# Optimization experiments

Measured on AMD Instinct MI355X. Metric: run time of the kernel, lower is better.

The kernel has to match this reference:

```python
import jax, jax.numpy as jnp
import numpy as np

EPS = 1e-6
NUM_HEADS = 16  # config.num_attention_heads

def _rms(h, w):
    h32 = h.astype(jnp.float32)
    v = jnp.mean(h32 * h32, axis=-1, keepdims=True)
    return (w * h32 * jax.lax.rsqrt(v + EPS)).astype(h.dtype)

def _rope(q, k, pos):
    dh = q.shape[-1]
    inv = 1.0 / (10000.0 ** (jnp.arange(0, dh, 2, dtype=jnp.float32) / dh))
    ang = pos.astype(jnp.float32)[:, None] * inv[None, :]  # [n, dh/2]
    cos = jnp.concatenate([jnp.cos(ang), jnp.cos(ang)], -1)[None, None]  # [1,1,n,dh]
    sin = jnp.concatenate([jnp.sin(ang), jnp.sin(ang)], -1)[None, None]
    def rot(x):
        x1, x2 = x[..., :dh // 2], x[..., dh // 2:]
        return jnp.concatenate([-x2, x1], -1)
    return q * cos + rot(q) * sin, k * cos + rot(k) * sin

def _skip_causal_mask(N, block_size, len1, text_len):
    qi = jnp.arange(N)[:, None]
    ki = jnp.arange(N)[None, :]
    qb = (qi - text_len) // block_size
    kb = (ki - text_len) // block_size
    iq = qi >= text_len
    ik = ki >= text_len
    return (((ki < text_len) & (qi >= ki))
            | (iq & ik & (qb < len1) & (kb < len1) & (qb >= kb))
            | (iq & ik & (qb >= len1) & (kb < len1) & (qb - len1 > kb))
            | (iq & ik & (qb == kb)))

def _layer(x, position_ids, text_position_ids, qkv_w, qkv_b, proj_w, proj_b,
           qn_w, kn_w, ln1_w, ln2_w, gate_w, up_w, down_w,
           block_size, text_len, len1):
    B, N, C = x.shape
    H = NUM_HEADS
    Dh = C // H
    T = text_len
    Lc = len1 * block_size
    offs = [0, T, T + Lc]
    lens = [T, Lc, N - T - Lc]  # text / clean / noised segment lengths
    qs, ks, vs = [], [], []
    for i in range(3):
        seg = _rms(x[:, offs[i]:offs[i] + lens[i]], ln1_w[i])  # input layernorm
        qkv = seg @ qkv_w[i] + qkv_b[i]                        # [B,n,3C]
        qkv = qkv.reshape(B, lens[i], 3, H, Dh).transpose(2, 0, 3, 1, 4)
        qs.append(_rms(qkv[0], qn_w[i]))
        ks.append(_rms(qkv[1], kn_w[i]))
        vs.append(qkv[2])
    img_q = jnp.concatenate([qs[1], qs[2]], axis=2)
    img_k = jnp.concatenate([ks[1], ks[2]], axis=2)
    img_q, img_k = _rope(img_q, img_k, position_ids)
    txt_q, txt_k = _rope(qs[0], ks[0], text_position_ids)
    q = jnp.concatenate([txt_q, img_q], axis=2)
    k = jnp.concatenate([txt_k, img_k], axis=2)
    v = jnp.concatenate(vs, axis=2)
    scores = jnp.einsum('bhqd,bhkd->bhqk', q, k) / np.float32(np.sqrt(Dh))
    mask = _skip_causal_mask(N, block_size, len1, text_len)
    scores = jnp.where(mask, scores, jnp.finfo(scores.dtype).min)
    attn = jax.nn.softmax(scores, axis=-1)
    o = jnp.einsum('bhqk,bhkd->bhqd', attn, v)
    o = o.transpose(0, 2, 1, 3).reshape(B, N, C)
    o = jnp.concatenate([o[:, offs[i]:offs[i] + lens[i]] @ proj_w[i] + proj_b[i]
                         for i in range(3)], axis=1)
    h = x + o
    mlp = []
    for i in range(3):
        y = _rms(h[:, offs[i]:offs[i] + lens[i]], ln2_w[i])  # post-attn layernorm
        mlp.append((jax.nn.silu(y @ gate_w[i]) * (y @ up_w[i])) @ down_w[i])
    return h + jnp.concatenate(mlp, axis=1)

def setup_inputs():
    key = jax.random.key(0)
    ks = jax.random.split(key, 8)
    B, C, H, I = 2, 1024, 16, 4096
    block_size, text_len, len1, len2 = 128, 256, 4, 4
    N = text_len + (len1 + len2) * block_size  # 1280
    s = 0.02
    return {
        'x': jax.random.normal(ks[0], (B, N, C), jnp.float32),
        'position_ids': jnp.arange((len1 + len2) * block_size, dtype=jnp.int32),
        'text_position_ids': jnp.arange(text_len, dtype=jnp.int32),
        'qkv_w': jax.random.normal(ks[1], (3, C, 3 * C), jnp.float32) * s,
        'qkv_b': jnp.zeros((3, 3 * C), jnp.float32),
        'proj_w': jax.random.normal(ks[2], (3, C, C), jnp.float32) * s,
        'proj_b': jnp.zeros((3, C), jnp.float32),
        'qn_w': jnp.ones((3, C // H), jnp.float32),
        'kn_w': jnp.ones((3, C // H), jnp.float32),
        'ln1_w': jnp.ones((3, C), jnp.float32),
        'ln2_w': jnp.ones((3, C), jnp.float32),
        'gate_w': jax.random.normal(ks[3], (3, C, I), jnp.float32) * s,
        'up_w': jax.random.normal(ks[4], (3, C, I), jnp.float32) * s,
        'down_w': jax.random.normal(ks[5], (3, I, C), jnp.float32) * s,
        'block_size': block_size, 'text_len': text_len, 'len1': len1,
    }

def reference(x, position_ids, text_position_ids, qkv_w, qkv_b, proj_w, proj_b,
              qn_w, kn_w, ln1_w, ln2_w, gate_w, up_w, down_w,
              block_size, text_len, len1):
    return _layer(x, position_ids, text_position_ids, qkv_w, qkv_b, proj_w, proj_b,
                  qn_w, kn_w, ln1_w, ln2_w, gate_w, up_w, down_w,
                  block_size, text_len, len1)
```

## Files before the change

### kernel.cpp

```cpp
#include <hip/hip_runtime.h>
#include <math.h>

constexpr int Bb  = 2;
constexpr int Nn  = 1280;
constexpr int Cc  = 1024;
constexpr int Hh  = 16;
constexpr int DH  = 64;
constexpr int Ii  = 4096;
constexpr int Tt  = 256;
constexpr int BSz = 128;
constexpr int L1  = 4;
constexpr int Mrows = Bb * Nn;

typedef __attribute__((ext_vector_type(8))) short short8v;
typedef __attribute__((ext_vector_type(4))) float f32x4;

__device__ __forceinline__ int segof(int n) {
    return n < Tt ? 0 : (n < Tt + L1 * BSz ? 1 : 2);
}
__device__ __forceinline__ unsigned short f2bf(float f) {
    unsigned int u = __float_as_uint(f);
    u += 0x7fffu + ((u >> 16) & 1u);
    return (unsigned short)(u >> 16);
}
__device__ __forceinline__ float bf2f(unsigned short h) {
    return __uint_as_float(((unsigned int)h) << 16);
}

__device__ __forceinline__ int xcd_swz(int lin, int nwg) {
    int cpx = nwg >> 3;
    return (lin & 7) * cpx + (lin >> 3);
}

__global__ __launch_bounds__(256)
void rms_bf16(const float* __restrict__ in, const float* __restrict__ w,
              unsigned short* __restrict__ out) {
    int row = blockIdx.x;
    int n   = row % Nn;
    int seg = segof(n);
    const float* x = in + (size_t)row * Cc;
    int t = threadIdx.x;
    float4 xv = reinterpret_cast<const float4*>(x)[t];
    float ss = xv.x * xv.x + xv.y * xv.y + xv.z * xv.z + xv.w * xv.w;
#pragma unroll
    for (int off = 32; off; off >>= 1) ss += __shfl_down(ss, off, 64);
    __shared__ float red[4];
    __shared__ float s_r;
    int lane = t & 63, wid = t >> 6;
    if (lane == 0) red[wid] = ss;
    __syncthreads();
    if (t == 0) s_r = rsqrtf((red[0] + red[1] + red[2] + red[3]) * (1.0f / Cc) + 1e-6f);
    __syncthreads();
    float r = s_r;
    float4 wv = reinterpret_cast<const float4*>(w + (size_t)seg * Cc)[t];
    ushort4 ov;
    ov.x = f2bf(wv.x * xv.x * r);
    ov.y = f2bf(wv.y * xv.y * r);
    ov.z = f2bf(wv.z * xv.z * r);
    ov.w = f2bf(wv.w * xv.w * r);
    *reinterpret_cast<ushort4*>(&out[(size_t)row * Cc + t * 4]) = ov;
}

__global__ __launch_bounds__(256)
void pack_w(const float* __restrict__ W, unsigned short* __restrict__ PB,
            int K, int Nd) {
    size_t idx = (size_t)blockIdx.x * 256 + threadIdx.x;
    size_t cpseg = (size_t)K * Nd / 8;
    int s = (int)(idx / cpseg);
    size_t rm = idx % cpseg;
    int lane = (int)(rm & 63);
    int fr   = (int)((rm >> 6) & 7);
    size_t tile = rm >> 9;
    int nct = Nd >> 7;
    int cb = (int)(tile % nct);
    int kt = (int)(tile / nct);
    int col = cb * 128 + fr * 16 + (lane & 15);
    int k0  = kt * 32 + (lane >> 4) * 8;
    const float* src = W + ((size_t)s * K + k0) * Nd + col;
    unsigned short o[8];
#pragma unroll
    for (int j = 0; j < 8; j++) o[j] = f2bf(src[(size_t)j * Nd]);
    short8v v;
#pragma unroll
    for (int j = 0; j < 8; j++) v[j] = (short)o[j];
    *reinterpret_cast<short8v*>(&PB[idx * 8]) = v;
}

template <int OUTMODE, bool BIAS, int NZ>
__global__ __launch_bounds__(256, 2)
void gemm128r(const unsigned short* __restrict__ A,
              const unsigned short* __restrict__ PB,
              const float* __restrict__ bias, void* __restrict__ outp,
              int K, int Nd) {
    __shared__ __align__(16) unsigned short lds[8192];
    int bx = blockIdx.x, by = blockIdx.y, bz = (NZ > 1) ? blockIdx.z : 0;
    {
        int gx = gridDim.x, gy = gridDim.y, gz = (NZ > 1) ? gridDim.z : 1;
        int lin = bx + gx * (by + gy * bz);
        int swz = xcd_swz(lin, gx * gy * gz);
        bx = swz % gx; swz /= gx;
        by = swz % gy; bz = swz / gy;
    }
    int rb = bx * 128, cb = by;
    int seg = segof(rb % Nn);
    int tid = threadIdx.x, lane = tid & 63, wid = tid >> 6;
    int wr = wid >> 1, wc = wid & 1;
    int g = lane >> 4, c_ = lane & 15;
    const int nct = Nd >> 7;
    const int Keff = K / NZ;
    const int nKt = Keff >> 5;
    const int kz = bz * Keff;
    const unsigned short* PBseg = PB + (size_t)seg * K * Nd;

    int mf0 = tid >> 6, lc0 = tid & 63;
    const unsigned short* pA0 =
        A + (size_t)(rb + mf0 * 16 + (lc0 & 15)) * K + kz + (lc0 >> 4) * 8;
    const unsigned short* pA1 = pA0 + (size_t)64 * K;
    const unsigned short* pB0 =
        PBseg + (((size_t)(kz >> 5) * nct + cb) * 8 + mf0) * 512 + (size_t)lc0 * 8;
    const unsigned short* pB1 = pB0 + 2048;
    const size_t bstep = (size_t)nct * 4096;

    f32x4 acc[4][4];
#pragma unroll
    for (int m = 0; m < 4; m++)
#pragma unroll
        for (int n = 0; n < 4; n++) acc[m][n] = (f32x4){0.f, 0.f, 0.f, 0.f};

    short8v av[2], bv[2];
    av[0] = *reinterpret_cast<const short8v*>(pA0);
    av[1] = *reinterpret_cast<const short8v*>(pA1);
    bv[0] = *reinterpret_cast<const short8v*>(pB0);
    bv[1] = *reinterpret_cast<const short8v*>(pB1);
    pA0 += 32; pA1 += 32; pB0 += bstep; pB1 += bstep;

    for (int kt = 0; kt < nKt; ++kt) {
        __syncthreads();
        *reinterpret_cast<short8v*>(&lds[(size_t)tid * 8]) = av[0];
        *reinterpret_cast<short8v*>(&lds[(size_t)(tid + 256) * 8]) = av[1];
        *reinterpret_cast<short8v*>(&lds[4096 + (size_t)tid * 8]) = bv[0];
        *reinterpret_cast<short8v*>(&lds[4096 + (size_t)(tid + 256) * 8]) = bv[1];
        __syncthreads();
        if (kt + 1 < nKt) {
            av[0] = *reinterpret_cast<const short8v*>(pA0);
            av[1] = *reinterpret_cast<const short8v*>(pA1);
            bv[0] = *reinterpret_cast<const short8v*>(pB0);
            bv[1] = *reinterpret_cast<const short8v*>(pB1);
            pA0 += 32; pA1 += 32; pB0 += bstep; pB1 += bstep;
        }
        short8v afr[4], bfr[4];
#pragma unroll
        for (int m = 0; m < 4; m++)
            afr[m] = *reinterpret_cast<short8v*>(&lds[((wr * 4 + m) * 64 + lane) * 8]);
#pragma unroll
        for (int n = 0; n < 4; n++)
            bfr[n] = *reinterpret_cast<short8v*>(&lds[4096 + ((wc * 4 + n) * 64 + lane) * 8]);
#pragma unroll
        for (int m = 0; m < 4; m++)
#pragma unroll
            for (int n = 0; n < 4; n++)
                acc[m][n] = __builtin_amdgcn_mfma_f32_16x16x32_bf16(
                    afr[m], bfr[n], acc[m][n], 0, 0, 0);
    }

    float* outf = (float*)outp;
    unsigned short* outh = (unsigned short*)outp;
    size_t zoff = (NZ > 1) ? (size_t)bz * Mrows * Nd : 0;
#pragma unroll
    for (int n = 0; n < 4; n++) {
        int col = cb * 128 + wc * 64 + n * 16 + c_;
        float bvv = BIAS ? bias[(size_t)seg * Nd + col] : 0.f;
#pragma unroll
        for (int m = 0; m < 4; m++) {
#pragma unroll
            for (int r = 0; r < 4; r++) {
                int row = rb + wr * 64 + m * 16 + g * 4 + r;
                float v = acc[m][n][r] + bvv;
                if (OUTMODE == 0) outf[zoff + (size_t)row * Nd + col] = v;
                else              outh[zoff + (size_t)row * Nd + col] = f2bf(v);
            }
        }
    }
}

__global__ __launch_bounds__(256, 2)
void gemm_gu(const unsigned short* __restrict__ A,
             const unsigned short* __restrict__ PG,
             const unsigned short* __restrict__ PU,
             unsigned short* __restrict__ outp) {
    __shared__ __align__(16) unsigned short lds[12288];
    int bx = blockIdx.x, by = blockIdx.y;
    {
        int lin = bx + gridDim.x * by;
        int swz = xcd_swz(lin, gridDim.x * gridDim.y);
        bx = swz % gridDim.x; by = swz / gridDim.x;
    }
    int rb = bx * 128, cb = by;
    int seg = segof(rb % Nn);
    int tid = threadIdx.x, lane = tid & 63, wid = tid >> 6;
    int wr = wid >> 1, wc = wid & 1;
    int g = lane >> 4, c_ = lane & 15;
    const int nct = Ii >> 7;
    const unsigned short* PGseg = PG + (size_t)seg * Cc * Ii;
    const unsigned short* PUseg = PU + (size_t)seg * Cc * Ii;

    int mf0 = tid >> 6, lc0 = tid & 63;
    const unsigned short* pA0 =
        A + (size_t)(rb + mf0 * 16 + (lc0 & 15)) * Cc + (lc0 >> 4) * 8;
    const unsigned short* pA1 = pA0 + (size_t)64 * Cc;
    size_t boff = ((size_t)cb * 8 + mf0) * 512 + (size_t)lc0 * 8;
    const unsigned short* pG0 = PGseg + boff;
    const unsigned short* pG1 = pG0 + 2048;
    const unsigned short* pU0 = PUseg + boff;
    const unsigned short* pU1 = pU0 + 2048;
    const size_t bstep = (size_t)nct * 4096;

    f32x4 accG[4][4], accU[4][4];
#pragma unroll
    for (int m = 0; m < 4; m++)
#pragma unroll
        for (int n = 0; n < 4; n++) {
            accG[m][n] = (f32x4){0.f, 0.f, 0.f, 0.f};
            accU[m][n] = (f32x4){0.f, 0.f, 0.f, 0.f};
        }

    short8v av[2], gv[2], uv[2];
    av[0] = *reinterpret_cast<const short8v*>(pA0);
    av[1] = *reinterpret_cast<const short8v*>(pA1);
    gv[0] = *reinterpret_cast<const short8v*>(pG0);
    gv[1] = *reinterpret_cast<const short8v*>(pG1);
    uv[0] = *reinterpret_cast<const short8v*>(pU0);
    uv[1] = *reinterpret_cast<const short8v*>(pU1);
    pA0 += 32; pA1 += 32; pG0 += bstep; pG1 += bstep; pU0 += bstep; pU1 += bstep;

    const int nKt = Cc >> 5;
    for (int kt = 0; kt < nKt; ++kt) {
        __syncthreads();
        *reinterpret_cast<short8v*>(&lds[(size_t)tid * 8]) = av[0];
        *reinterpret_cast<short8v*>(&lds[(size_t)(tid + 256) * 8]) = av[1];
        *reinterpret_cast<short8v*>(&lds[4096 + (size_t)tid * 8]) = gv[0];
        *reinterpret_cast<short8v*>(&lds[4096 + (size_t)(tid + 256) * 8]) = gv[1];
        *reinterpret_cast<short8v*>(&lds[8192 + (size_t)tid * 8]) = uv[0];
        *reinterpret_cast<short8v*>(&lds[8192 + (size_t)(tid + 256) * 8]) = uv[1];
        __syncthreads();
        if (kt + 1 < nKt) {
            av[0] = *reinterpret_cast<const short8v*>(pA0);
            av[1] = *reinterpret_cast<const short8v*>(pA1);
            gv[0] = *reinterpret_cast<const short8v*>(pG0);
            gv[1] = *reinterpret_cast<const short8v*>(pG1);
            uv[0] = *reinterpret_cast<const short8v*>(pU0);
            uv[1] = *reinterpret_cast<const short8v*>(pU1);
            pA0 += 32; pA1 += 32; pG0 += bstep; pG1 += bstep; pU0 += bstep; pU1 += bstep;
        }
        short8v afr[4];
#pragma unroll
        for (int m = 0; m < 4; m++)
            afr[m] = *reinterpret_cast<short8v*>(&lds[((wr * 4 + m) * 64 + lane) * 8]);
        {
            short8v gfr[4];
#pragma unroll
            for (int n = 0; n < 4; n++)
                gfr[n] = *reinterpret_cast<short8v*>(&lds[4096 + ((wc * 4 + n) * 64 + lane) * 8]);
#pragma unroll
            for (int m = 0; m < 4; m++)
#pragma unroll
                for (int n = 0; n < 4; n++)
                    accG[m][n] = __builtin_amdgcn_mfma_f32_16x16x32_bf16(
                        afr[m], gfr[n], accG[m][n], 0, 0, 0);
        }
        {
            short8v ufr[4];
#pragma unroll
            for (int n = 0; n < 4; n++)
                ufr[n] = *reinterpret_cast<short8v*>(&lds[8192 + ((wc * 4 + n) * 64 + lane) * 8]);
#pragma unroll
            for (int m = 0; m < 4; m++)
#pragma unroll
                for (int n = 0; n < 4; n++)
                    accU[m][n] = __builtin_amdgcn_mfma_f32_16x16x32_bf16(
                        afr[m], ufr[n], accU[m][n], 0, 0, 0);
        }
    }

#pragma unroll
    for (int n = 0; n < 4; n++) {
        int col = cb * 128 + wc * 64 + n * 16 + c_;
#pragma unroll
        for (int m = 0; m < 4; m++) {
#pragma unroll
            for (int r = 0; r < 4; r++) {
                int row = rb + wr * 64 + m * 16 + g * 4 + r;
                float gval = accG[m][n][r], uval = accU[m][n][r];
                float t = gval / (1.f + __expf(-gval)) * uval;
                outp[(size_t)row * Ii + col] = f2bf(t);
            }
        }
    }
}

__global__ __launch_bounds__(256)
void combine_proj(const float* __restrict__ x, const float* __restrict__ bias,
                  const float* __restrict__ p, float* __restrict__ hb) {
    int i = blockIdx.x * 256 + threadIdx.x;
    int base = i * 4;
    int col = base % Cc;
    int n   = (base / Cc) % Nn;
    int seg = segof(n);
    float4 a = reinterpret_cast<const float4*>(x)[i];
    float4 b = *reinterpret_cast<const float4*>(&bias[(size_t)seg * Cc + col]);
    float4 p0 = reinterpret_cast<const float4*>(p)[i];
    float4 p1 = reinterpret_cast<const float4*>(p)[i + Mrows * Cc / 4];
    float4 r;
    r.x = a.x + b.x + p0.x + p1.x;
    r.y = a.y + b.y + p0.y + p1.y;
    r.z = a.z + b.z + p0.z + p1.z;
    r.w = a.w + b.w + p0.w + p1.w;
    reinterpret_cast<float4*>(hb)[i] = r;
}

__global__ __launch_bounds__(256)
void combine_down4(const unsigned short* __restrict__ p,
                   float* __restrict__ out) {
    int i = blockIdx.x * 256 + threadIdx.x;
    float4 a = reinterpret_cast<const float4*>(out)[i];
#pragma unroll
    for (int z = 0; z < 4; z++) {
        ushort4 u = *reinterpret_cast<const ushort4*>(&p[(size_t)z * Mrows * Cc + i * 4]);
        a.x += bf2f(u.x); a.y += bf2f(u.y); a.z += bf2f(u.z); a.w += bf2f(u.w);
    }
    reinterpret_cast<float4*>(out)[i] = a;
}

__global__ __launch_bounds__(256)
void split_rope(const unsigned short* __restrict__ qkv,
                const float* __restrict__ qn_w, const float* __restrict__ kn_w,
                const int* __restrict__ pos_ids, const int* __restrict__ tpos_ids,
                unsigned short* __restrict__ Q, unsigned short* __restrict__ K,
                unsigned short* __restrict__ V) {
    int row = blockIdx.x;
    int b = row / Nn, n = row % Nn;
    int seg = segof(n);
    int lane = threadIdx.x & 63, wid = threadIdx.x >> 6;
    int pos = (n < Tt) ? tpos_ids[n] : pos_ids[n - Tt];
    int j = lane & 31;
    float ang = (float)pos * exp2f(-(float)j * (13.287712379549449f / 32.f));
    float cv = cosf(ang), sv = sinf(ang);
    float qw = qn_w[seg * DH + lane], kw = kn_w[seg * DH + lane];
    for (int h = wid; h < Hh; h += 4) {
        const unsigned short* base = qkv + (size_t)row * (3 * Cc) + h * DH + lane;
        float q = bf2f(base[0]), k = bf2f(base[Cc]), v = bf2f(base[2 * Cc]);
        float qs = q * q, ks = k * k;
#pragma unroll
        for (int off = 32; off; off >>= 1) {
            qs += __shfl_xor(qs, off, 64);
            ks += __shfl_xor(ks, off, 64);
        }
        q = q * rsqrtf(qs * (1.f / DH) + 1e-6f) * qw;
        k = k * rsqrtf(ks * (1.f / DH) + 1e-6f) * kw;
        float qp = __shfl_xor(q, 32, 64);
        float kp = __shfl_xor(k, 32, 64);
        float qo = q * cv + ((lane < 32) ? -qp * sv : qp * sv);
        float ko = k * cv + ((lane < 32) ? -kp * sv : kp * sv);
        size_t oidx = ((size_t)(b * Hh + h) * Nn + n) * DH + lane;
        Q[oidx] = f2bf(qo);
        K[oidx] = f2bf(ko);
        V[oidx] = f2bf(v);
    }
}

__global__ __launch_bounds__(256)
void attn_mfma(const unsigned short* __restrict__ Qg,
               const unsigned short* __restrict__ Kg,
               const unsigned short* __restrict__ Vg,
               unsigned short* __restrict__ O) {
    __shared__ __align__(16) unsigned short k_lds[64 * 64];
    __shared__ __align__(16) unsigned short vt_lds[64 * 64];
    __shared__ __align__(16) unsigned short p_lds[4][16 * 64];

    int qt = blockIdx.x;
    int bh = blockIdx.y;
    int b = bh >> 4, h = bh & 15;
    int tid = threadIdx.x, lane = tid & 63, wid = tid >> 6;
    int g = lane >> 4, c = lane & 15;

    const size_t headoff = (size_t)bh * Nn * DH;
    int q0 = qt * 64;
    bool qtext = q0 < Tt;
    int qb = qtext ? 0 : (q0 - Tt) / BSz;

    int qrow_frag = q0 + wid * 16 + c;
    short8v aq[2];
#pragma unroll
    for (int kb = 0; kb < 2; kb++)
        aq[kb] = *reinterpret_cast<const short8v*>(
            &Qg[headoff + (size_t)qrow_frag * DH + kb * 32 + g * 8]);

    unsigned short* pbuf = &p_lds[wid][0];

    f32x4 o_[4];
#pragma unroll
    for (int nb = 0; nb < 4; nb++) o_[nb] = (f32x4){0.f, 0.f, 0.f, 0.f};
    float m_[4] = {-3.4e38f, -3.4e38f, -3.4e38f, -3.4e38f};
    float l_[4] = {0.f, 0.f, 0.f, 0.f};

    int tr = tid >> 2, tc = tid & 3;

    for (int kt = 0; kt < Nn / 64; kt++) {
        int kbase = kt * 64;
        bool vis, diag = false;
        if (qtext) {
            vis = (kbase <= q0);
            diag = (kbase == q0);
        } else if (kbase < Tt) {
            vis = true;
        } else {
            int kb = (kbase - Tt) / BSz;
            vis = (qb < L1) ? (kb <= qb)
                            : ((kb < L1 && qb - L1 > kb) || kb == qb);
        }
        if (!vis) continue;

        __syncthreads();
        {
            const unsigned short* ks = &Kg[headoff + (size_t)(kbase + tr) * DH];
            const unsigned short* vs = &Vg[headoff + (size_t)(kbase + tr) * DH];
#pragma unroll
            for (int i = 0; i < 2; i++) {
                int ch = tc + i * 4;
                short8v kv = *reinterpret_cast<const short8v*>(ks + ch * 8);
                int byte = (tr * 128 + ch * 16) ^ ((tr & 7) << 4);
                *reinterpret_cast<short8v*>((char*)k_lds + byte) = kv;
                short8v vv = *reinterpret_cast<const short8v*>(vs + ch * 8);
#pragma unroll
                for (int j = 0; j < 8; j++) {
                    int dh = ch * 8 + j;
                    int vbyte = (dh * 128 + tr * 2) ^ ((dh & 7) << 4);
                    *reinterpret_cast<unsigned short*>((char*)vt_lds + vbyte) =
                        (unsigned short)vv[j];
                }
            }
        }
        __syncthreads();

        f32x4 s_[4];
#pragma unroll
        for (int nb = 0; nb < 4; nb++) s_[nb] = (f32x4){0.f, 0.f, 0.f, 0.f};
#pragma unroll
        for (int nb = 0; nb < 4; nb++) {
            int kil = nb * 16 + c;
#pragma unroll
            for (int kb = 0; kb < 2; kb++) {
                int byte = (kil * 128 + kb * 64 + g * 16) ^ ((kil & 7) << 4);
                short8v bk = *reinterpret_cast<short8v*>((char*)k_lds + byte);
                s_[nb] = __builtin_amdgcn_mfma_f32_16x16x32_bf16(aq[kb], bk, s_[nb], 0, 0, 0);
            }
        }
#pragma unroll
        for (int nb = 0; nb < 4; nb++) {
#pragma unroll
            for (int r = 0; r < 4; r++) {
                float sv = s_[nb][r] * 0.125f;
                if (diag) {
                    int qrl = wid * 16 + g * 4 + r;
                    int kcl = nb * 16 + c;
                    if (qrl < kcl) sv = -3.4e38f;
                }
                s_[nb][r] = sv;
            }
        }
#pragma unroll
        for (int r = 0; r < 4; r++) {
            float mx = fmaxf(fmaxf(s_[0][r], s_[1][r]), fmaxf(s_[2][r], s_[3][r]));
#pragma unroll
            for (int off = 1; off <= 8; off <<= 1)
                mx = fmaxf(mx, __shfl_xor(mx, off, 64));
            float mn = fmaxf(m_[r], mx);
            float es = __expf(m_[r] - mn);
            m_[r] = mn;
            float pv[4];
            float rs = 0.f;
#pragma unroll
            for (int nb = 0; nb < 4; nb++) {
                pv[nb] = __expf(s_[nb][r] - mn);
                rs += pv[nb];
            }
#pragma unroll
            for (int off = 1; off <= 8; off <<= 1)
                rs += __shfl_xor(rs, off, 64);
            l_[r] = l_[r] * es + rs;
#pragma unroll
            for (int nb = 0; nb < 4; nb++) o_[nb][r] *= es;
            int qrl = g * 4 + r;
            int swz = (qrl & 7) << 4;
#pragma unroll
            for (int nb = 0; nb < 4; nb++) {
                int byte = (qrl * 128 + (nb * 16 + c) * 2) ^ swz;
                *reinterpret_cast<unsigned short*>((char*)pbuf + byte) = f2bf(pv[nb]);
            }
        }
        short8v aP[2];
#pragma unroll
        for (int kb = 0; kb < 2; kb++) {
            int byte = (c * 128 + kb * 64 + g * 16) ^ ((c & 7) << 4);
            aP[kb] = *reinterpret_cast<short8v*>((char*)pbuf + byte);
        }
#pragma unroll
        for (int nb = 0; nb < 4; nb++) {
            int dh = nb * 16 + c;
#pragma unroll
            for (int kb = 0; kb < 2; kb++) {
                int byte = (dh * 128 + kb * 64 + g * 16) ^ ((dh & 7) << 4);
                short8v bv = *reinterpret_cast<short8v*>((char*)vt_lds + byte);
                o_[nb] = __builtin_amdgcn_mfma_f32_16x16x32_bf16(aP[kb], bv, o_[nb], 0, 0, 0);
            }
        }
    }

    float inv_[4];
#pragma unroll
    for (int r = 0; r < 4; r++) inv_[r] = 1.f / l_[r];
#pragma unroll
    for (int nb = 0; nb < 4; nb++) {
        int col = h * DH + nb * 16 + c;
#pragma unroll
        for (int r = 0; r < 4; r++) {
            int row = q0 + wid * 16 + g * 4 + r;
            O[((size_t)b * Nn + row) * Cc + col] = f2bf(o_[nb][r] * inv_[r]);
        }
    }
}

extern "C" void kernel_launch(void* const* d_in, const int* in_sizes, int n_in,
                              void* d_out, int out_size, void* d_ws, size_t ws_size,
                              hipStream_t stream) {
    const float* x        = (const float*)d_in[0];
    const int*   pos_ids  = (const int*)d_in[1];
    const int*   tpos_ids = (const int*)d_in[2];
    const float* qkv_w    = (const float*)d_in[3];
    const float* qkv_b    = (const float*)d_in[4];
    const float* proj_w   = (const float*)d_in[5];
    const float* proj_b   = (const float*)d_in[6];
    const float* qn_w     = (const float*)d_in[7];
    const float* kn_w     = (const float*)d_in[8];
    const float* ln1_w    = (const float*)d_in[9];
    const float* ln2_w    = (const float*)d_in[10];
    const float* gate_w   = (const float*)d_in[11];
    const float* up_w     = (const float*)d_in[12];
    const float* down_w   = (const float*)d_in[13];
    float* out = (float*)d_out;
    char*  wsb = (char*)d_ws;

    unsigned short* WA  = (unsigned short*)(wsb);
    unsigned short* WB  = (unsigned short*)(wsb + 25165824);
    unsigned short* Tb  = (unsigned short*)(wsb + 50331648);
    unsigned short* P3  = (unsigned short*)(wsb + 71303168);
    unsigned short* Qbf = Tb;
    unsigned short* Kbf = Tb + 2621440;
    unsigned short* Vbf = Tb + 5242880;

    rms_bf16<<<Mrows, 256, 0, stream>>>(x, ln1_w, P3);
    pack_w<<<4608, 256, 0, stream>>>(qkv_w, WA, Cc, 3 * Cc);
    gemm128r<1, true, 1><<<dim3(Mrows / 128, 24), 256, 0, stream>>>(
        P3, WA, qkv_b, WB, Cc, 3 * Cc);
    split_rope<<<Mrows, 256, 0, stream>>>(WB, qn_w, kn_w, pos_ids, tpos_ids,
                                          Qbf, Kbf, Vbf);
    attn_mfma<<<dim3(Nn / 64, Bb * Hh), 256, 0, stream>>>(Qbf, Kbf, Vbf, P3);
    pack_w<<<1536, 256, 0, stream>>>(proj_w, WA, Cc, Cc);
    gemm128r<0, false, 2><<<dim3(Mrows / 128, 8, 2), 256, 0, stream>>>(
        P3, WA, nullptr, (float*)Tb, Cc, Cc);
    combine_proj<<<Mrows * Cc / 1024, 256, 0, stream>>>(x, proj_b, (float*)Tb, out);
    rms_bf16<<<Mrows, 256, 0, stream>>>(out, ln2_w, P3);
    pack_w<<<6144, 256, 0, stream>>>(gate_w, WA, Cc, Ii);
    pack_w<<<6144, 256, 0, stream>>>(up_w, WB, Cc, Ii);
    gemm_gu<<<dim3(Mrows / 128, 32), 256, 0, stream>>>(P3, WA, WB, Tb);
    pack_w<<<6144, 256, 0, stream>>>(down_w, WA, Ii, Cc);
    gemm128r<1, false, 4><<<dim3(Mrows / 128, 8, 4), 256, 0, stream>>>(
        Tb, WA, nullptr, WB, Ii, Cc);
    combine_down4<<<Mrows * Cc / 1024, 256, 0, stream>>>(WB, out);
}
```

Measured before the change: 275.2 us.

## Fuse fp32-to-bf16 weight packing into GEMM tile loads, drop pack kernels

Removes the separate pack_w kernels that converted fp32 weights to a tiled bf16 layout. Each GEMM now reads fp32 weights directly, converts them with packed v_cvt_pk_bf16_f32 and writes them to LDS in the MFMA fragment order. This saves five launches plus a full write and reread of the converted weights, and the workspace is re-laid out to match. In exchange each weight element is reloaded and reconverted by every row-block (20 of them). The loads are also strided: 8 rows apart per thread, 16 consecutive floats per row, and fp32 doubles the bytes per load.

Result: slower. 299.2 us (+8.7%).

```diff
diff --git a/kernel.cpp b/kernel.cpp
--- a/kernel.cpp
+++ b/kernel.cpp
@@ -25,6 +25,17 @@
 }
 __device__ __forceinline__ float bf2f(unsigned short h) {
     return __uint_as_float(((unsigned int)h) << 16);
+}
+__device__ __forceinline__ unsigned int cvtpk(float lo, float hi) {
+    unsigned int r;
+    asm("v_cvt_pk_bf16_f32 %0, %1, %2" : "=v"(r) : "v"(lo), "v"(hi));
+    return r;
+}
+__device__ __forceinline__ uint4 pk8(const float* w) {
+    uint4 r;
+    r.x = cvtpk(w[0], w[1]); r.y = cvtpk(w[2], w[3]);
+    r.z = cvtpk(w[4], w[5]); r.w = cvtpk(w[6], w[7]);
+    return r;
 }
 
 __device__ __forceinline__ int xcd_swz(int lin, int nwg) {
@@ -61,35 +72,10 @@
     *reinterpret_cast<ushort4*>(&out[(size_t)row * Cc + t * 4]) = ov;
 }
 
-__global__ __launch_bounds__(256)
-void pack_w(const float* __restrict__ W, unsigned short* __restrict__ PB,
-            int K, int Nd) {
-    size_t idx = (size_t)blockIdx.x * 256 + threadIdx.x;
-    size_t cpseg = (size_t)K * Nd / 8;
-    int s = (int)(idx / cpseg);
-    size_t rm = idx % cpseg;
-    int lane = (int)(rm & 63);
-    int fr   = (int)((rm >> 6) & 7);
-    size_t tile = rm >> 9;
-    int nct = Nd >> 7;
-    int cb = (int)(tile % nct);
-    int kt = (int)(tile / nct);
-    int col = cb * 128 + fr * 16 + (lane & 15);
-    int k0  = kt * 32 + (lane >> 4) * 8;
-    const float* src = W + ((size_t)s * K + k0) * Nd + col;
-    unsigned short o[8];
-#pragma unroll
-    for (int j = 0; j < 8; j++) o[j] = f2bf(src[(size_t)j * Nd]);
-    short8v v;
-#pragma unroll
-    for (int j = 0; j < 8; j++) v[j] = (short)o[j];
-    *reinterpret_cast<short8v*>(&PB[idx * 8]) = v;
-}
-
 template <int OUTMODE, bool BIAS, int NZ>
 __global__ __launch_bounds__(256, 2)
 void gemm128r(const unsigned short* __restrict__ A,
-              const unsigned short* __restrict__ PB,
+              const float* __restrict__ W,
               const float* __restrict__ bias, void* __restrict__ outp,
               int K, int Nd) {
     __shared__ __align__(16) unsigned short lds[8192];
@@ -106,20 +92,18 @@
     int tid = threadIdx.x, lane = tid & 63, wid = tid >> 6;
     int wr = wid >> 1, wc = wid & 1;
     int g = lane >> 4, c_ = lane & 15;
-    const int nct = Nd >> 7;
     const int Keff = K / NZ;
     const int nKt = Keff >> 5;
     const int kz = bz * Keff;
-    const unsigned short* PBseg = PB + (size_t)seg * K * Nd;
 
     int mf0 = tid >> 6, lc0 = tid & 63;
     const unsigned short* pA0 =
         A + (size_t)(rb + mf0 * 16 + (lc0 & 15)) * K + kz + (lc0 >> 4) * 8;
     const unsigned short* pA1 = pA0 + (size_t)64 * K;
-    const unsigned short* pB0 =
-        PBseg + (((size_t)(kz >> 5) * nct + cb) * 8 + mf0) * 512 + (size_t)lc0 * 8;
-    const unsigned short* pB1 = pB0 + 2048;
-    const size_t bstep = (size_t)nct * 4096;
+    const float* pW0 = W + (size_t)seg * K * Nd +
+                       (size_t)(kz + (lc0 >> 4) * 8) * Nd +
+                       cb * 128 + mf0 * 16 + (lc0 & 15);
+    const size_t wstep = (size_t)32 * Nd;
 
     f32x4 acc[4][4];
 #pragma unroll
@@ -127,27 +111,31 @@
 #pragma unroll
         for (int n = 0; n < 4; n++) acc[m][n] = (f32x4){0.f, 0.f, 0.f, 0.f};
 
-    short8v av[2], bv[2];
-    av[0] = *reinterpret_cast<const short8v*>(pA0);
-    av[1] = *reinterpret_cast<const short8v*>(pA1);
-    bv[0] = *reinterpret_cast<const short8v*>(pB0);
-    bv[1] = *reinterpret_cast<const short8v*>(pB1);
-    pA0 += 32; pA1 += 32; pB0 += bstep; pB1 += bstep;
-
+    short8v av0, av1;
+    uint4 ub0, ub1;
+    auto load_tile = [&]() {
+        av0 = *reinterpret_cast<const short8v*>(pA0);
+        av1 = *reinterpret_cast<const short8v*>(pA1);
+        float w0[8], w1[8];
+#pragma unroll
+        for (int j = 0; j < 8; j++) {
+            w0[j] = pW0[(size_t)j * Nd];
+            w1[j] = pW0[(size_t)j * Nd + 64];
+        }
+        ub0 = pk8(w0);
+        ub1 = pk8(w1);
+        pA0 += 32; pA1 += 32; pW0 += wstep;
+    };
+
+    load_tile();
     for (int kt = 0; kt < nKt; ++kt) {
         __syncthreads();
-        *reinterpret_cast<short8v*>(&lds[(size_t)tid * 8]) = av[0];
-        *reinterpret_cast<short8v*>(&lds[(size_t)(tid + 256) * 8]) = av[1];
-        *reinterpret_cast<short8v*>(&lds[4096 + (size_t)tid * 8]) = bv[0];
-        *reinterpret_cast<short8v*>(&lds[4096 + (size_t)(tid + 256) * 8]) = bv[1];
+        *reinterpret_cast<short8v*>(&lds[(size_t)tid * 8]) = av0;
+        *reinterpret_cast<short8v*>(&lds[(size_t)(tid + 256) * 8]) = av1;
+        *reinterpret_cast<uint4*>(&lds[4096 + (size_t)tid * 8]) = ub0;
+        *reinterpret_cast<uint4*>(&lds[4096 + (size_t)(tid + 256) * 8]) = ub1;
         __syncthreads();
-        if (kt + 1 < nKt) {
-            av[0] = *reinterpret_cast<const short8v*>(pA0);
-            av[1] = *reinterpret_cast<const short8v*>(pA1);
-            bv[0] = *reinterpret_cast<const short8v*>(pB0);
-            bv[1] = *reinterpret_cast<const short8v*>(pB1);
-            pA0 += 32; pA1 += 32; pB0 += bstep; pB1 += bstep;
-        }
+        if (kt + 1 < nKt) load_tile();
         short8v afr[4], bfr[4];
 #pragma unroll
         for (int m = 0; m < 4; m++)
@@ -185,8 +173,8 @@
 
 __global__ __launch_bounds__(256, 2)
 void gemm_gu(const unsigned short* __restrict__ A,
-             const unsigned short* __restrict__ PG,
-             const unsigned short* __restrict__ PU,
+             const float* __restrict__ G,
+             const float* __restrict__ U,
              unsigned short* __restrict__ outp) {
     __shared__ __align__(16) unsigned short lds[12288];
     int bx = blockIdx.x, by = blockIdx.y;
@@ -200,20 +188,16 @@
     int tid = threadIdx.x, lane = tid & 63, wid = tid >> 6;
     int wr = wid >> 1, wc = wid & 1;
     int g = lane >> 4, c_ = lane & 15;
-    const int nct = Ii >> 7;
-    const unsigned short* PGseg = PG + (size_t)seg * Cc * Ii;
-    const unsigned short* PUseg = PU + (size_t)seg * Cc * Ii;
 
     int mf0 = tid >> 6, lc0 = tid & 63;
     const unsigned short* pA0 =
         A + (size_t)(rb + mf0 * 16 + (lc0 & 15)) * Cc + (lc0 >> 4) * 8;
     const unsigned short* pA1 = pA0 + (size_t)64 * Cc;
-    size_t boff = ((size_t)cb * 8 + mf0) * 512 + (size_t)lc0 * 8;
-    const unsigned short* pG0 = PGseg + boff;
-    const unsigned short* pG1 = pG0 + 2048;
-    const unsigned short* pU0 = PUseg + boff;
-    const unsigned short* pU1 = pU0 + 2048;
-    const size_t bstep = (size_t)nct * 4096;
+    size_t wofs = (size_t)seg * Cc * Ii + (size_t)((lc0 >> 4) * 8) * Ii +
+                  cb * 128 + mf0 * 16 + (lc0 & 15);
+    const float* pG0 = G + wofs;
+    const float* pU0 = U + wofs;
+    const size_t wstep = (size_t)32 * Ii;
 
     f32x4 accG[4][4], accU[4][4];
 #pragma unroll
@@ -224,34 +208,36 @@
             accU[m][n] = (f32x4){0.f, 0.f, 0.f, 0.f};
         }
 
-    short8v av[2], gv[2], uv[2];
-    av[0] = *reinterpret_cast<const short8v*>(pA0);
-    av[1] = *reinterpret_cast<const short8v*>(pA1);
-    gv[0] = *reinterpret_cast<const short8v*>(pG0);
-    gv[1] = *reinterpret_cast<const short8v*>(pG1);
-    uv[0] = *reinterpret_cast<const short8v*>(pU0);
-    uv[1] = *reinterpret_cast<const short8v*>(pU1);
-    pA0 += 32; pA1 += 32; pG0 += bstep; pG1 += bstep; pU0 += bstep; pU1 += bstep;
+    short8v av0, av1;
+    uint4 gb0, gb1, ub0, ub1;
+    auto load_tile = [&]() {
+        av0 = *reinterpret_cast<const short8v*>(pA0);
+        av1 = *reinterpret_cast<const short8v*>(pA1);
+        float g0[8], g1[8], u0[8], u1[8];
+#pragma unroll
+        for (int j = 0; j < 8; j++) {
+            g0[j] = pG0[(size_t)j * Ii];
+            g1[j] = pG0[(size_t)j * Ii + 64];
+            u0[j] = pU0[(size_t)j * Ii];
+            u1[j] = pU0[(size_t)j * Ii + 64];
+        }
+        gb0 = pk8(g0); gb1 = pk8(g1);
+        ub0 = pk8(u0); ub1 = pk8(u1);
+        pA0 += 32; pA1 += 32; pG0 += wstep; pU0 += wstep;
+    };
 
     const int nKt = Cc >> 5;
+    load_tile();
     for (int kt = 0; kt < nKt; ++kt) {
         __syncthreads();
-        *reinterpret_cast<short8v*>(&lds[(size_t)tid * 8]) = av[0];
-        *reinterpret_cast<short8v*>(&lds[(size_t)(tid + 256) * 8]) = av[1];
-        *reinterpret_cast<short8v*>(&lds[4096 + (size_t)tid * 8]) = gv[0];
-        *reinterpret_cast<short8v*>(&lds[4096 + (size_t)(tid + 256) * 8]) = gv[1];
-        *reinterpret_cast<short8v*>(&lds[8192 + (size_t)tid * 8]) = uv[0];
-        *reinterpret_cast<short8v*>(&lds[8192 + (size_t)(tid + 256) * 8]) = uv[1];
+        *reinterpret_cast<short8v*>(&lds[(size_t)tid * 8]) = av0;
+        *reinterpret_cast<short8v*>(&lds[(size_t)(tid + 256) * 8]) = av1;
+        *reinterpret_cast<uint4*>(&lds[4096 + (size_t)tid * 8]) = gb0;
+        *reinterpret_cast<uint4*>(&lds[4096 + (size_t)(tid + 256) * 8]) = gb1;
+        *reinterpret_cast<uint4*>(&lds[8192 + (size_t)tid * 8]) = ub0;
+        *reinterpret_cast<uint4*>(&lds[8192 + (size_t)(tid + 256) * 8]) = ub1;
         __syncthreads();
-        if (kt + 1 < nKt) {
-            av[0] = *reinterpret_cast<const short8v*>(pA0);
-            av[1] = *reinterpret_cast<const short8v*>(pA1);
-            gv[0] = *reinterpret_cast<const short8v*>(pG0);
-            gv[1] = *reinterpret_cast<const short8v*>(pG1);
-            uv[0] = *reinterpret_cast<const short8v*>(pU0);
-            uv[1] = *reinterpret_cast<const short8v*>(pU1);
-            pA0 += 32; pA1 += 32; pG0 += bstep; pG1 += bstep; pU0 += bstep; pU1 += bstep;
-        }
+        if (kt + 1 < nKt) load_tile();
         short8v afr[4];
 #pragma unroll
         for (int m = 0; m < 4; m++)
@@ -550,31 +536,27 @@
     float* out = (float*)d_out;
     char*  wsb = (char*)d_ws;
 
-    unsigned short* WA  = (unsigned short*)(wsb);
-    unsigned short* WB  = (unsigned short*)(wsb + 25165824);
-    unsigned short* Tb  = (unsigned short*)(wsb + 50331648);
-    unsigned short* P3  = (unsigned short*)(wsb + 71303168);
-    unsigned short* Qbf = Tb;
-    unsigned short* Kbf = Tb + 2621440;
-    unsigned short* Vbf = Tb + 5242880;
+    unsigned short* P3   = (unsigned short*)(wsb);
+    unsigned short* qkvb = (unsigned short*)(wsb + 5242880);
+    unsigned short* Qbf  = (unsigned short*)(wsb + 20971520);
+    unsigned short* Kbf  = Qbf + 2621440;
+    unsigned short* Vbf  = Qbf + 5242880;
+    float*          Pp   = (float*)(wsb + 36700160);
+    unsigned short* Tb   = (unsigned short*)(wsb + 36700160);
+    unsigned short* Dp   = (unsigned short*)(wsb + 57671680);
 
     rms_bf16<<<Mrows, 256, 0, stream>>>(x, ln1_w, P3);
-    pack_w<<<4608, 256, 0, stream>>>(qkv_w, WA, Cc, 3 * Cc);
     gemm128r<1, true, 1><<<dim3(Mrows / 128, 24), 256, 0, stream>>>(
-        P3, WA, qkv_b, WB, Cc, 3 * Cc);
-    split_rope<<<Mrows, 256, 0, stream>>>(WB, qn_w, kn_w, pos_ids, tpos_ids,
+        P3, qkv_w, qkv_b, qkvb, Cc, 3 * Cc);
+    split_rope<<<Mrows, 256, 0, stream>>>(qkvb, qn_w, kn_w, pos_ids, tpos_ids,
                                           Qbf, Kbf, Vbf);
     attn_mfma<<<dim3(Nn / 64, Bb * Hh), 256, 0, stream>>>(Qbf, Kbf, Vbf, P3);
-    pack_w<<<1536, 256, 0, stream>>>(proj_w, WA, Cc, Cc);
     gemm128r<0, false, 2><<<dim3(Mrows / 128, 8, 2), 256, 0, stream>>>(
-        P3, WA, nullptr, (float*)Tb, Cc, Cc);
-    combine_proj<<<Mrows * Cc / 1024, 256, 0, stream>>>(x, proj_b, (float*)Tb, out);
+        P3, proj_w, nullptr, Pp, Cc, Cc);
+    combine_proj<<<Mrows * Cc / 1024, 256, 0, stream>>>(x, proj_b, Pp, out);
     rms_bf16<<<Mrows, 256, 0, stream>>>(out, ln2_w, P3);
-    pack_w<<<6144, 256, 0, stream>>>(gate_w, WA, Cc, Ii);
-    pack_w<<<6144, 256, 0, stream>>>(up_w, WB, Cc, Ii);
-    gemm_gu<<<dim3(Mrows / 128, 32), 256, 0, stream>>>(P3, WA, WB, Tb);
-    pack_w<<<6144, 256, 0, stream>>>(down_w, WA, Ii, Cc);
+    gemm_gu<<<dim3(Mrows / 128, 32), 256, 0, stream>>>(P3, gate_w, up_w, Tb);
     gemm128r<1, false, 4><<<dim3(Mrows / 128, 8, 4), 256, 0, stream>>>(
-        Tb, WA, nullptr, WB, Ii, Cc);
-    combine_down4<<<Mrows * Cc / 1024, 256, 0, stream>>>(WB, out);
-}
+        Tb, down_w, nullptr, Dp, Ii, Cc);
+    combine_down4<<<Mrows * Cc / 1024, 256, 0, stream>>>(Dp, out);
+}
```
